# Kernel tuning notes

Measured on AMD Instinct MI355X. Metric: run time of the kernel, lower is better.

## Reference

```python
import jax, jax.numpy as jnp
import numpy as np

H = 1024        # hidden_dim
MD = 2048       # memory_dim
L = 16384       # memory length == max_length
N = 8           # head_N
# sys.float_info.min underflows to 0.0 in float32, exactly as in the torch
# original (python float * float32 tensor). Kept for faithfulness.
TINY = jnp.float32(2.2250738585072014e-308)


def setup_inputs() -> dict:
    key = jax.random.key(0)
    ks = jax.random.split(key, 12)
    s_h = 1.0 / np.sqrt(H)
    s_m = 1.0 / np.sqrt(MD)
    s_o = 1.0 / np.sqrt(2 * H)
    return {
        "x": jax.random.normal(ks[0], (1, 1, H), jnp.float32),
        "memory": jax.random.normal(ks[1], (L, MD), jnp.float32),
        "Wq": jax.random.uniform(ks[2], (H, H), jnp.float32, -s_h, s_h),
        "bq": jax.random.uniform(ks[3], (H,), jnp.float32, -s_h, s_h),
        "Wk": jax.random.uniform(ks[4], (H, MD), jnp.float32, -s_m, s_m),
        "bk": jax.random.uniform(ks[5], (H,), jnp.float32, -s_m, s_m),
        "Wv": jax.random.uniform(ks[6], (H, MD), jnp.float32, -s_m, s_m),
        "bv": jax.random.uniform(ks[7], (H,), jnp.float32, -s_m, s_m),
        "Wo": jax.random.uniform(ks[8], (H, 2 * H), jnp.float32, -s_o, s_o),
        "bo": jax.random.uniform(ks[9], (H,), jnp.float32, -s_o, s_o),
    }


def reference(x, memory, Wq, bq, Wk, bk, Wv, bv, Wo, bo):
    d = H // N  # per-head dim
    # Q: (1,H) -> (1,d,N) -> (N,1,d), scaled by d**-0.5
    q = x.reshape(1, -1) @ Wq.T + bq
    Q = q.reshape(1, d, N).transpose(2, 0, 1) * (d ** -0.5)
    # K: (L,H) -> (L,d,N) -> (N,d,L)
    K = (memory @ Wk.T + bk).reshape(-1, d, N).transpose(2, 1, 0)
    QK = jnp.einsum('nod,ndl->nol', Q, K)  # (N,1,L)
    # pad mask: 1 where the memory row sums to zero, else 0 (as in torch nonzero-set)
    any_zero = memory.sum(axis=1)
    pad_mask = (any_zero == 0).astype(QK.dtype)[None, None, :]
    QK = QK + pad_mask * TINY
    attn = jax.nn.softmax(QK, axis=-1)
    # V: (L,H) -> (L,d,N) -> (N,L,d)
    V = (memory @ Wv.T + bv).reshape(-1, d, N).transpose(2, 0, 1)
    feat = jnp.einsum('nol,nld->nod', attn, V)      # (N,1,d)
    feat = feat.transpose(1, 2, 0).reshape(1, 1, H)  # (1,1,H)
    ax = jnp.concatenate([x, feat], axis=-1)         # (1,1,2H)
    return jax.nn.relu(ax @ Wo.T + bo)
```

## Files before the change

### kernel.cpp

```cpp
#include <hip/hip_runtime.h>
#include <math.h>

#define LROWS 16384
#define HDIM  1024
#define MDIM  2048
#define NH    8
#define RSQRT_D 0.08838834764831844f

#define OFF_W     0
#define OFF_BETA  16384
#define OFF_Z     16392
#define OFF_Q     16400
#define OFF_FEAT  17424
#define OFF_Y     18448
#define OFF_S2    34832
#define OFF_YBUF  296976

__device__ __forceinline__ float dot4(float4 a, float4 b) {
  return a.x * b.x + a.y * b.y + a.z * b.z + a.w * b.w;
}
__device__ __forceinline__ void fma4(float4& acc, float s, float4 v) {
  acc.x = fmaf(s, v.x, acc.x); acc.y = fmaf(s, v.y, acc.y);
  acc.z = fmaf(s, v.z, acc.z); acc.w = fmaf(s, v.w, acc.w);
}
__device__ __forceinline__ void add4(float4& a, float4 v) {
  a.x += v.x; a.y += v.y; a.z += v.z; a.w += v.w;
}

__global__ __launch_bounds__(256) void k1_q(const float* __restrict__ x,
                                            const float* __restrict__ Wq,
                                            const float* __restrict__ bq,
                                            const float* __restrict__ bk,
                                            float* __restrict__ ws) {
  int tid = threadIdx.x, lane = tid & 63;
  int j = blockIdx.x * 4 + (tid >> 6);
  const float4* xr = (const float4*)x;
  const float4* wr = (const float4*)(Wq + (size_t)j * HDIM);
  float acc = 0.f;
#pragma unroll
  for (int i = 0; i < 4; ++i) {
    int idx = i * 64 + lane;
    acc += dot4(xr[idx], wr[idx]);
  }
#pragma unroll
  for (int off = 32; off; off >>= 1) acc += __shfl_xor(acc, off);
  if (lane == 0) {
    float qj = acc + bq[j];
    ws[OFF_Q + j] = qj;
    atomicAdd(&ws[OFF_BETA + (j & 7)], qj * bk[j]);
  }
}

__global__ __launch_bounds__(256) void k2_w(const float* __restrict__ Wk,
                                            float* __restrict__ ws) {
  int tid = threadIdx.x;
  int mc = blockIdx.x & 7, cc = blockIdx.x >> 3;
  int m = mc * 256 + tid;
  const float* q = ws + OFF_Q;
  float acc[8];
#pragma unroll
  for (int n = 0; n < 8; ++n) acc[n] = 0.f;
  int c0 = cc * 32;
#pragma unroll
  for (int cb = 0; cb < 32; cb += 8) {
#pragma unroll
    for (int u = 0; u < 8; ++u)
      acc[u] = fmaf(q[c0 + cb + u], Wk[(size_t)(c0 + cb + u) * MDIM + m], acc[u]);
  }
#pragma unroll
  for (int n = 0; n < 8; ++n) atomicAdd(&ws[OFF_W + n * MDIM + m], acc[n]);
}

__global__ __launch_bounds__(256, 4) void kA2(const float* __restrict__ mem,
                                              float* __restrict__ ws) {
  __shared__ float4 wlds[2048];
  int tid = threadIdx.x, lane = tid & 63, wv = tid >> 6;
  int rg = blockIdx.x >> 1, ch = blockIdx.x & 1;
  int r0 = rg * 16;

  const float4* wsrc = (const float4*)(ws + OFF_W + ch * 1024);
#pragma unroll
  for (int k = 0; k < 8; ++k) {
    int qi = k * 256 + tid;
    int n = qi >> 8, c4 = qi & 255;
    wlds[qi] = wsrc[n * 512 + c4];
  }
  __syncthreads();

  float acc[4][8];
#pragma unroll
  for (int rr = 0; rr < 4; ++rr)
#pragma unroll
    for (int n = 0; n < 8; ++n) acc[rr][n] = 0.f;

  const size_t cbase = (size_t)ch * 1024;
  float4 mv[4], mvn[4];
#pragma unroll
  for (int rr = 0; rr < 4; ++rr)
    mv[rr] = *(const float4*)(mem + (size_t)(r0 + wv * 4 + rr) * MDIM + cbase + (size_t)lane * 4);

#pragma unroll
  for (int step = 0; step < 4; ++step) {
    int cq = step * 64 + lane;
    float4 wvv[8];
#pragma unroll
    for (int n = 0; n < 8; ++n) wvv[n] = wlds[n * 256 + cq];
    if (step < 3) {
#pragma unroll
      for (int rr = 0; rr < 4; ++rr)
        mvn[rr] = *(const float4*)(mem + (size_t)(r0 + wv * 4 + rr) * MDIM + cbase + (size_t)(cq + 64) * 4);
    }
#pragma unroll
    for (int rr = 0; rr < 4; ++rr) {
#pragma unroll
      for (int n = 0; n < 8; ++n) {
        acc[rr][n] = fmaf(mv[rr].x, wvv[n].x, acc[rr][n]);
        acc[rr][n] = fmaf(mv[rr].y, wvv[n].y, acc[rr][n]);
        acc[rr][n] = fmaf(mv[rr].z, wvv[n].z, acc[rr][n]);
        acc[rr][n] = fmaf(mv[rr].w, wvv[n].w, acc[rr][n]);
      }
    }
#pragma unroll
    for (int rr = 0; rr < 4; ++rr) mv[rr] = mvn[rr];
  }

#pragma unroll
  for (int off = 1; off < 64; off <<= 1) {
#pragma unroll
    for (int rr = 0; rr < 4; ++rr)
#pragma unroll
      for (int n = 0; n < 8; ++n)
        acc[rr][n] += __shfl_xor(acc[rr][n], off);
  }
  if (lane == 0) {
    float* sdst = ws + OFF_S2 + (size_t)ch * 131072 + (size_t)(r0 + wv * 4) * 8;
#pragma unroll
    for (int rr = 0; rr < 4; ++rr)
#pragma unroll
      for (int n = 0; n < 8; ++n)
        sdst[rr * 8 + n] = acc[rr][n];
  }
}

__global__ __launch_bounds__(256, 4) void kB2(const float* __restrict__ mem,
                                              float* __restrict__ ws) {
  __shared__ __align__(16) float pp[256];
  __shared__ float zz[32];
  int tid = threadIdx.x;
  int rc = blockIdx.x >> 1, ch = blockIdx.x & 1;
  int r0 = rc * 32;
  {
    int n = tid & 7;
    int r = r0 + (tid >> 3);
    float s0 = ws[OFF_S2 + (size_t)r * 8 + n];
    float s1 = ws[OFF_S2 + 131072 + (size_t)r * 8 + n];
    float p = __expf((s0 + s1 + ws[OFF_BETA + n]) * RSQRT_D);
    pp[tid] = p;
    if (ch == 0) {
      float z = p;
      z += __shfl_xor(z, 8); z += __shfl_xor(z, 16); z += __shfl_xor(z, 32);
      if ((tid & 63) < 8) zz[(tid >> 6) * 8 + n] = z;
    }
  }
  __syncthreads();
  if (ch == 0 && tid < 8)
    atomicAdd(&ws[OFF_Z + tid], zz[tid] + zz[8 + tid] + zz[16 + tid] + zz[24 + tid]);

  float4 acc[8];
#pragma unroll
  for (int n = 0; n < 8; ++n) acc[n] = make_float4(0.f, 0.f, 0.f, 0.f);

  const float* base = mem + (size_t)r0 * MDIM + ch * 1024 + tid * 4;
#pragma unroll 4
  for (int r = 0; r < 32; ++r) {
    float4 mv = *(const float4*)(base + (size_t)r * MDIM);
    float4 pA = *(const float4*)(pp + r * 8);
    float4 pB = *(const float4*)(pp + r * 8 + 4);
    fma4(acc[0], pA.x, mv); fma4(acc[1], pA.y, mv);
    fma4(acc[2], pA.z, mv); fma4(acc[3], pA.w, mv);
    fma4(acc[4], pB.x, mv); fma4(acc[5], pB.y, mv);
    fma4(acc[6], pB.z, mv); fma4(acc[7], pB.w, mv);
  }
  float* yb = ws + OFF_YBUF + (size_t)rc * 16384 + ch * 1024 + tid * 4;
#pragma unroll
  for (int n = 0; n < 8; ++n)
    *(float4*)(yb + n * MDIM) = acc[n];
}

__global__ __launch_bounds__(256) void k4c(float* __restrict__ ws) {
  __shared__ float4 sA[256];
  int t = threadIdx.x;
  int quad = blockIdx.x * 16 + (t & 15);
  int b0 = (t >> 4) * 32;
  const float4* src = (const float4*)(ws + OFF_YBUF);
  float4 acc = make_float4(0.f, 0.f, 0.f, 0.f);
  for (int b = b0; b < b0 + 32; ++b)
    add4(acc, src[(size_t)b * 4096 + quad]);
  sA[(t & 15) * 16 + (t >> 4)] = acc;
  __syncthreads();
  if (t < 16) {
    float4 s = sA[t * 16];
#pragma unroll
    for (int j = 1; j < 16; ++j) add4(s, sA[t * 16 + j]);
    ((float4*)(ws + OFF_Y))[blockIdx.x * 16 + t] = s;
  }
}

__global__ __launch_bounds__(256) void k6_feat(const float* __restrict__ Wv,
                                               const float* __restrict__ bv,
                                               float* __restrict__ ws) {
  int tid = threadIdx.x, lane = tid & 63;
  int c = blockIdx.x * 4 + (tid >> 6);
  int n = c & 7;
  const float4* yb = (const float4*)(ws + OFF_Y + n * MDIM);
  const float4* wb = (const float4*)(Wv + (size_t)c * MDIM);
  float acc = 0.f;
#pragma unroll
  for (int s = 0; s < 8; ++s) {
    int idx = s * 64 + lane;
    acc += dot4(yb[idx], wb[idx]);
  }
#pragma unroll
  for (int off = 32; off; off >>= 1) acc += __shfl_xor(acc, off);
  if (lane == 0) ws[OFF_FEAT + c] = acc / ws[OFF_Z + n] + bv[c];
}

__global__ __launch_bounds__(256) void k7_out(const float* __restrict__ x,
                                              const float* __restrict__ Wo,
                                              const float* __restrict__ bo,
                                              const float* __restrict__ ws,
                                              float* __restrict__ out) {
  int tid = threadIdx.x, lane = tid & 63;
  int j = blockIdx.x * 4 + (tid >> 6);
  const float4* wb = (const float4*)(Wo + (size_t)j * 2048);
  const float4* xr = (const float4*)x;
  const float4* fr = (const float4*)(ws + OFF_FEAT);
  float acc = 0.f;
#pragma unroll
  for (int s = 0; s < 4; ++s) {
    int idx = s * 64 + lane;
    acc += dot4(xr[idx], wb[idx]);
    acc += dot4(fr[idx], wb[256 + idx]);
  }
#pragma unroll
  for (int off = 32; off; off >>= 1) acc += __shfl_xor(acc, off);
  if (lane == 0) out[j] = fmaxf(acc + bo[j], 0.f);
}

extern "C" void kernel_launch(void* const* d_in, const int* in_sizes, int n_in,
                              void* d_out, int out_size, void* d_ws, size_t ws_size,
                              hipStream_t stream) {
  const float* x   = (const float*)d_in[0];
  const float* mem = (const float*)d_in[1];
  const float* Wq  = (const float*)d_in[2];
  const float* bq  = (const float*)d_in[3];
  const float* Wk  = (const float*)d_in[4];
  const float* bk  = (const float*)d_in[5];
  const float* Wv  = (const float*)d_in[6];
  const float* bv  = (const float*)d_in[7];
  const float* Wo  = (const float*)d_in[8];
  const float* bo  = (const float*)d_in[9];
  float* ws  = (float*)d_ws;
  float* out = (float*)d_out;

  hipMemsetAsync(ws, 0, OFF_Q * sizeof(float), stream);

  k1_q   <<<256, 256, 0, stream>>>(x, Wq, bq, bk, ws);
  k2_w   <<<256, 256, 0, stream>>>(Wk, ws);
  kA2    <<<2048, 256, 0, stream>>>(mem, ws);
  kB2    <<<1024, 256, 0, stream>>>(mem, ws);
  k4c    <<<256, 256, 0, stream>>>(ws);
  k6_feat<<<256, 256, 0, stream>>>(Wv, bv, ws);
  k7_out <<<256, 256, 0, stream>>>(x, Wo, bo, ws, out);
}
```

Before: 289.0 us.

## Drop memset and atomics, restructure score kernel and Y reduction

Removes the hipMemsetAsync by zeroing the W accumulator inside the Q kernel, and computes beta in a dedicated extra block instead of with atomics. The score kernel now has each wave walk 8 rows sequentially with a per-row shuffle reduction, halving the grid, and it reloads W from LDS on every pass rather than keeping it in registers. The Z normalizer is written as per-block partials and reduced later, and the Y-buffer reduction is re-split over 1024 blocks with shuffle-based reductions. The aim is to cut launch and atomic overhead and raise parallelism in the reduction, at the cost of more LDS reads and more shuffles per row in the score kernel.

```diff
diff --git a/kernel.cpp b/kernel.cpp
--- a/kernel.cpp
+++ b/kernel.cpp
@@ -4,7 +4,6 @@
 #define LROWS 16384
 #define HDIM  1024
 #define MDIM  2048
-#define NH    8
 #define RSQRT_D 0.08838834764831844f
 
 #define OFF_W     0
@@ -13,8 +12,9 @@
 #define OFF_Q     16400
 #define OFF_FEAT  17424
 #define OFF_Y     18448
-#define OFF_S2    34832
-#define OFF_YBUF  296976
+#define OFF_ZP    34832
+#define OFF_S2    38928
+#define OFF_YBUF  301072
 
 __device__ __forceinline__ float dot4(float4 a, float4 b) {
   return a.x * b.x + a.y * b.y + a.z * b.z + a.w * b.w;
@@ -27,11 +27,10 @@
   a.x += v.x; a.y += v.y; a.z += v.z; a.w += v.w;
 }
 
-__global__ __launch_bounds__(256) void k1_q(const float* __restrict__ x,
-                                            const float* __restrict__ Wq,
-                                            const float* __restrict__ bq,
-                                            const float* __restrict__ bk,
-                                            float* __restrict__ ws) {
+__global__ __launch_bounds__(256) void kq(const float* __restrict__ x,
+                                          const float* __restrict__ Wq,
+                                          const float* __restrict__ bq,
+                                          float* __restrict__ ws) {
   int tid = threadIdx.x, lane = tid & 63;
   int j = blockIdx.x * 4 + (tid >> 6);
   const float4* xr = (const float4*)x;
@@ -44,19 +43,32 @@
   }
 #pragma unroll
   for (int off = 32; off; off >>= 1) acc += __shfl_xor(acc, off);
-  if (lane == 0) {
-    float qj = acc + bq[j];
-    ws[OFF_Q + j] = qj;
-    atomicAdd(&ws[OFF_BETA + (j & 7)], qj * bk[j]);
-  }
-}
-
-__global__ __launch_bounds__(256) void k2_w(const float* __restrict__ Wk,
-                                            float* __restrict__ ws) {
+  if (lane == 0) ws[OFF_Q + j] = acc + bq[j];
+  if (tid < 64) ws[OFF_W + blockIdx.x * 64 + tid] = 0.f;
+}
+
+__global__ __launch_bounds__(256) void kw(const float* __restrict__ Wk,
+                                          const float* __restrict__ bk,
+                                          float* __restrict__ ws) {
+  __shared__ float lds[32];
   int tid = threadIdx.x;
+  const float* q = ws + OFF_Q;
+  if (blockIdx.x == 256) {
+    float b = 0.f;
+#pragma unroll
+    for (int i = 0; i < 4; ++i) {
+      int c = tid + 256 * i;
+      b = fmaf(q[c], bk[c], b);
+    }
+    b += __shfl_xor(b, 8); b += __shfl_xor(b, 16); b += __shfl_xor(b, 32);
+    if ((tid & 63) < 8) lds[(tid >> 6) * 8 + (tid & 7)] = b;
+    __syncthreads();
+    if (tid < 8)
+      ws[OFF_BETA + tid] = lds[tid] + lds[8 + tid] + lds[16 + tid] + lds[24 + tid];
+    return;
+  }
   int mc = blockIdx.x & 7, cc = blockIdx.x >> 3;
   int m = mc * 256 + tid;
-  const float* q = ws + OFF_Q;
   float acc[8];
 #pragma unroll
   for (int n = 0; n < 8; ++n) acc[n] = 0.f;
@@ -71,82 +83,70 @@
   for (int n = 0; n < 8; ++n) atomicAdd(&ws[OFF_W + n * MDIM + m], acc[n]);
 }
 
-__global__ __launch_bounds__(256, 4) void kA2(const float* __restrict__ mem,
+__global__ __launch_bounds__(256, 4) void kA3(const float* __restrict__ mem,
                                               float* __restrict__ ws) {
   __shared__ float4 wlds[2048];
   int tid = threadIdx.x, lane = tid & 63, wv = tid >> 6;
-  int rg = blockIdx.x >> 1, ch = blockIdx.x & 1;
-  int r0 = rg * 16;
-
+  int ch = blockIdx.x & 1, rg = blockIdx.x >> 1;
   const float4* wsrc = (const float4*)(ws + OFF_W + ch * 1024);
 #pragma unroll
   for (int k = 0; k < 8; ++k) {
     int qi = k * 256 + tid;
-    int n = qi >> 8, c4 = qi & 255;
-    wlds[qi] = wsrc[n * 512 + c4];
+    wlds[qi] = wsrc[(qi >> 8) * 512 + (qi & 255)];
   }
   __syncthreads();
 
-  float acc[4][8];
-#pragma unroll
-  for (int rr = 0; rr < 4; ++rr)
-#pragma unroll
-    for (int n = 0; n < 8; ++n) acc[rr][n] = 0.f;
-
-  const size_t cbase = (size_t)ch * 1024;
+  int r0 = rg * 32 + wv * 8;
+  const float* base = mem + (size_t)r0 * MDIM + ch * 1024;
+  float* sbase = ws + OFF_S2 + (size_t)ch * 131072 + (size_t)r0 * 8;
+
   float4 mv[4], mvn[4];
 #pragma unroll
-  for (int rr = 0; rr < 4; ++rr)
-    mv[rr] = *(const float4*)(mem + (size_t)(r0 + wv * 4 + rr) * MDIM + cbase + (size_t)lane * 4);
-
-#pragma unroll
-  for (int step = 0; step < 4; ++step) {
-    int cq = step * 64 + lane;
-    float4 wvv[8];
-#pragma unroll
-    for (int n = 0; n < 8; ++n) wvv[n] = wlds[n * 256 + cq];
-    if (step < 3) {
-#pragma unroll
-      for (int rr = 0; rr < 4; ++rr)
-        mvn[rr] = *(const float4*)(mem + (size_t)(r0 + wv * 4 + rr) * MDIM + cbase + (size_t)(cq + 64) * 4);
-    }
-#pragma unroll
-    for (int rr = 0; rr < 4; ++rr) {
+  for (int i = 0; i < 4; ++i)
+    mv[i] = *(const float4*)(base + (i * 64 + lane) * 4);
+
+#pragma unroll
+  for (int rl = 0; rl < 8; ++rl) {
+    if (rl < 7) {
+#pragma unroll
+      for (int i = 0; i < 4; ++i)
+        mvn[i] = *(const float4*)(base + (size_t)(rl + 1) * MDIM + (i * 64 + lane) * 4);
+    }
+    float acc[8];
+#pragma unroll
+    for (int n = 0; n < 8; ++n) acc[n] = 0.f;
+#pragma unroll
+    for (int pass = 0; pass < 4; ++pass) {
+      int cq = pass * 64 + lane;
 #pragma unroll
       for (int n = 0; n < 8; ++n) {
-        acc[rr][n] = fmaf(mv[rr].x, wvv[n].x, acc[rr][n]);
-        acc[rr][n] = fmaf(mv[rr].y, wvv[n].y, acc[rr][n]);
-        acc[rr][n] = fmaf(mv[rr].z, wvv[n].z, acc[rr][n]);
-        acc[rr][n] = fmaf(mv[rr].w, wvv[n].w, acc[rr][n]);
+        float4 w4 = wlds[n * 256 + cq];
+        acc[n] = fmaf(mv[pass].x, w4.x, acc[n]);
+        acc[n] = fmaf(mv[pass].y, w4.y, acc[n]);
+        acc[n] = fmaf(mv[pass].z, w4.z, acc[n]);
+        acc[n] = fmaf(mv[pass].w, w4.w, acc[n]);
       }
     }
 #pragma unroll
-    for (int rr = 0; rr < 4; ++rr) mv[rr] = mvn[rr];
-  }
-
-#pragma unroll
-  for (int off = 1; off < 64; off <<= 1) {
-#pragma unroll
-    for (int rr = 0; rr < 4; ++rr)
+    for (int off = 1; off < 64; off <<= 1)
 #pragma unroll
       for (int n = 0; n < 8; ++n)
-        acc[rr][n] += __shfl_xor(acc[rr][n], off);
-  }
-  if (lane == 0) {
-    float* sdst = ws + OFF_S2 + (size_t)ch * 131072 + (size_t)(r0 + wv * 4) * 8;
-#pragma unroll
-    for (int rr = 0; rr < 4; ++rr)
-#pragma unroll
-      for (int n = 0; n < 8; ++n)
-        sdst[rr * 8 + n] = acc[rr][n];
-  }
-}
-
-__global__ __launch_bounds__(256, 4) void kB2(const float* __restrict__ mem,
-                                              float* __restrict__ ws) {
+        acc[n] += __shfl_xor(acc[n], off);
+    if (lane == 0) {
+      float4* dst = (float4*)(sbase + rl * 8);
+      dst[0] = make_float4(acc[0], acc[1], acc[2], acc[3]);
+      dst[1] = make_float4(acc[4], acc[5], acc[6], acc[7]);
+    }
+#pragma unroll
+    for (int i = 0; i < 4; ++i) mv[i] = mvn[i];
+  }
+}
+
+__global__ __launch_bounds__(256, 4) void kb(const float* __restrict__ mem,
+                                             float* __restrict__ ws) {
   __shared__ __align__(16) float pp[256];
   __shared__ float zz[32];
-  int tid = threadIdx.x;
+  int tid = threadIdx.x, lane = tid & 63, wv = tid >> 6;
   int rc = blockIdx.x >> 1, ch = blockIdx.x & 1;
   int r0 = rc * 32;
   {
@@ -159,23 +159,22 @@
     if (ch == 0) {
       float z = p;
       z += __shfl_xor(z, 8); z += __shfl_xor(z, 16); z += __shfl_xor(z, 32);
-      if ((tid & 63) < 8) zz[(tid >> 6) * 8 + n] = z;
+      if (lane < 8) zz[wv * 8 + lane] = z;
     }
   }
   __syncthreads();
   if (ch == 0 && tid < 8)
-    atomicAdd(&ws[OFF_Z + tid], zz[tid] + zz[8 + tid] + zz[16 + tid] + zz[24 + tid]);
+    ws[OFF_ZP + rc * 8 + tid] = zz[tid] + zz[8 + tid] + zz[16 + tid] + zz[24 + tid];
 
   float4 acc[8];
 #pragma unroll
   for (int n = 0; n < 8; ++n) acc[n] = make_float4(0.f, 0.f, 0.f, 0.f);
-
   const float* base = mem + (size_t)r0 * MDIM + ch * 1024 + tid * 4;
+  const float4* pp4 = (const float4*)pp;
 #pragma unroll 4
   for (int r = 0; r < 32; ++r) {
     float4 mv = *(const float4*)(base + (size_t)r * MDIM);
-    float4 pA = *(const float4*)(pp + r * 8);
-    float4 pB = *(const float4*)(pp + r * 8 + 4);
+    float4 pA = pp4[r * 2], pB = pp4[r * 2 + 1];
     fma4(acc[0], pA.x, mv); fma4(acc[1], pA.y, mv);
     fma4(acc[2], pA.z, mv); fma4(acc[3], pA.w, mv);
     fma4(acc[4], pB.x, mv); fma4(acc[5], pB.y, mv);
@@ -187,28 +186,50 @@
     *(float4*)(yb + n * MDIM) = acc[n];
 }
 
-__global__ __launch_bounds__(256) void k4c(float* __restrict__ ws) {
-  __shared__ float4 sA[256];
-  int t = threadIdx.x;
-  int quad = blockIdx.x * 16 + (t & 15);
-  int b0 = (t >> 4) * 32;
+__global__ __launch_bounds__(256) void ky(float* __restrict__ ws) {
+  __shared__ __align__(16) float lds[96];
+  int tid = threadIdx.x, lane = tid & 63, wv = tid >> 6;
+  int bid = blockIdx.x;
   const float4* src = (const float4*)(ws + OFF_YBUF);
-  float4 acc = make_float4(0.f, 0.f, 0.f, 0.f);
-  for (int b = b0; b < b0 + 32; ++b)
-    add4(acc, src[(size_t)b * 4096 + quad]);
-  sA[(t & 15) * 16 + (t >> 4)] = acc;
+  int qd = bid * 4 + (tid & 3);
+  int h = tid >> 2;
+  float4 a = make_float4(0.f, 0.f, 0.f, 0.f);
+#pragma unroll
+  for (int i = 0; i < 8; ++i)
+    add4(a, src[(size_t)(h + 64 * i) * 4096 + qd]);
+#pragma unroll
+  for (int off = 4; off < 64; off <<= 1) {
+    a.x += __shfl_xor(a.x, off);
+    a.y += __shfl_xor(a.y, off);
+    a.z += __shfl_xor(a.z, off);
+    a.w += __shfl_xor(a.w, off);
+  }
+  float4* sq = (float4*)lds;
+  if (lane < 4) sq[wv * 4 + lane] = a;
   __syncthreads();
-  if (t < 16) {
-    float4 s = sA[t * 16];
-#pragma unroll
-    for (int j = 1; j < 16; ++j) add4(s, sA[t * 16 + j]);
-    ((float4*)(ws + OFF_Y))[blockIdx.x * 16 + t] = s;
-  }
-}
-
-__global__ __launch_bounds__(256) void k6_feat(const float* __restrict__ Wv,
-                                               const float* __restrict__ bv,
-                                               float* __restrict__ ws) {
+  if (tid < 4) {
+    float4 s = sq[tid];
+    add4(s, sq[4 + tid]); add4(s, sq[8 + tid]); add4(s, sq[12 + tid]);
+    ((float4*)(ws + OFF_Y))[bid * 4 + tid] = s;
+  }
+  if (bid == 0) {
+    int n = tid & 7;
+    float z = 0.f;
+#pragma unroll
+    for (int i = 0; i < 16; ++i)
+      z += ws[OFF_ZP + ((tid >> 3) + 32 * i) * 8 + n];
+    z += __shfl_xor(z, 8); z += __shfl_xor(z, 16); z += __shfl_xor(z, 32);
+    float* zzz = lds + 64;
+    if (lane < 8) zzz[wv * 8 + lane] = z;
+    __syncthreads();
+    if (tid < 8)
+      ws[OFF_Z + tid] = zzz[tid] + zzz[8 + tid] + zzz[16 + tid] + zzz[24 + tid];
+  }
+}
+
+__global__ __launch_bounds__(256) void kf(const float* __restrict__ Wv,
+                                          const float* __restrict__ bv,
+                                          float* __restrict__ ws) {
   int tid = threadIdx.x, lane = tid & 63;
   int c = blockIdx.x * 4 + (tid >> 6);
   int n = c & 7;
@@ -225,11 +246,11 @@
   if (lane == 0) ws[OFF_FEAT + c] = acc / ws[OFF_Z + n] + bv[c];
 }
 
-__global__ __launch_bounds__(256) void k7_out(const float* __restrict__ x,
-                                              const float* __restrict__ Wo,
-                                              const float* __restrict__ bo,
-                                              const float* __restrict__ ws,
-                                              float* __restrict__ out) {
+__global__ __launch_bounds__(256) void ko(const float* __restrict__ x,
+                                          const float* __restrict__ Wo,
+                                          const float* __restrict__ bo,
+                                          const float* __restrict__ ws,
+                                          float* __restrict__ out) {
   int tid = threadIdx.x, lane = tid & 63;
   int j = blockIdx.x * 4 + (tid >> 6);
   const float4* wb = (const float4*)(Wo + (size_t)j * 2048);
@@ -263,13 +284,11 @@
   float* ws  = (float*)d_ws;
   float* out = (float*)d_out;
 
-  hipMemsetAsync(ws, 0, OFF_Q * sizeof(float), stream);
-
-  k1_q   <<<256, 256, 0, stream>>>(x, Wq, bq, bk, ws);
-  k2_w   <<<256, 256, 0, stream>>>(Wk, ws);
-  kA2    <<<2048, 256, 0, stream>>>(mem, ws);
-  kB2    <<<1024, 256, 0, stream>>>(mem, ws);
-  k4c    <<<256, 256, 0, stream>>>(ws);
-  k6_feat<<<256, 256, 0, stream>>>(Wv, bv, ws);
-  k7_out <<<256, 256, 0, stream>>>(x, Wo, bo, ws, out);
-}
+  kq <<<256,  256, 0, stream>>>(x, Wq, bq, ws);
+  kw <<<257,  256, 0, stream>>>(Wk, bk, ws);
+  kA3<<<1024, 256, 0, stream>>>(mem, ws);
+  kb <<<1024, 256, 0, stream>>>(mem, ws);
+  ky <<<1024, 256, 0, stream>>>(ws);
+  kf <<<256,  256, 0, stream>>>(Wv, bv, ws);
+  ko <<<256,  256, 0, stream>>>(x, Wo, bo, ws, out);
+}
```

New measurement: 273.9 us. 5.2% less time.
